# Kernel tuning notes

Measured on AMD Instinct MI355X. Metric: run time of the kernel, lower is better.

Reference implementation:

```python
import jax, jax.numpy as jnp
import numpy as np


def rational_hat(points, centers, radius):
    # points: [B, P, 2], centers: [K, 2], radius: [1]
    # L1 distance of each point to each center: [B, P, K]
    norm = jnp.abs(points[:, :, None, :] - centers[None, None, :, :]).sum(-1)
    r = jnp.abs(radius[0])
    val = 1.0 / (1.0 + norm) - 1.0 / (1.0 + jnp.abs(r - norm))
    return val.sum(axis=1)  # [B, K]


def setup_inputs() -> dict:
    key = jax.random.key(0)
    k1, k2, k3, k4, k5 = jax.random.split(key, 5)
    B, N0, N1, N2, K = 32, 20000, 10000, 10000, 64
    return {
        "beta_0_up": jax.random.uniform(k1, (B, N0, 2), dtype=jnp.float32),
        "beta_0_down": jax.random.uniform(k2, (B, N0, 2), dtype=jnp.float32),
        "beta0_ext": jax.random.uniform(k3, (B, N1, 2), dtype=jnp.float32),
        "beta1_ext": jax.random.uniform(k4, (B, N2, 2), dtype=jnp.float32),
        "centers": jax.random.uniform(k5, (K, 2), dtype=jnp.float32),
        "radius": jnp.full((1,), 0.1, dtype=jnp.float32),
    }


def reference(beta_0_up, beta_0_down, beta0_ext, beta1_ext, centers, radius):
    x0, y0 = beta0_ext[..., 0], beta0_ext[..., 1]
    x1, y1 = beta1_ext[..., 0], beta1_ext[..., 1]
    b0_1st = jnp.stack([x0, 1.0 - x0], axis=-1)  # [B, N1, 2]
    b0_2nd = jnp.stack([y0, 1.0 - y0], axis=-1)
    b1_1st = jnp.stack([x1, 1.0 - x1], axis=-1)  # [B, N2, 2]
    b1_2nd = jnp.stack([y1, 1.0 - y1], axis=-1)
    ph_down = jnp.concatenate([beta_0_down, b0_1st, b1_1st], axis=1)  # [B, P, 2]
    ph_up = jnp.concatenate([beta_0_up, b0_2nd, b1_2nd], axis=1)
    up_out = rational_hat(ph_up, centers, radius)    # [B, K]
    down_out = rational_hat(ph_down, centers, radius)
    tpl = -((up_out - down_out) ** 2).sum()
    x = jnp.concatenate([up_out, down_out], axis=1)  # [B, 2K]
    return (x, tpl)
```

## Files before the change

### kernel.cpp

```cpp
#include <hip/hip_runtime.h>

typedef float v2f __attribute__((ext_vector_type(2)));

#define NB 32
#define N0 20000
#define N1 10000
#define N2 10000
#define NT_A 157
#define KC_A 8
#define KC_B 16
#define NBINS 4096
#define SENT 3.0e4f

__global__ __launch_bounds__(256, 8) void hat_kernel(
    const float* __restrict__ up0, const float* __restrict__ down0,
    const float* __restrict__ ext0, const float* __restrict__ ext1,
    const float* __restrict__ centers, const float* __restrict__ radius,
    float* __restrict__ out)
{
    const int tid  = threadIdx.x;
    const int lane = tid & 63;
    const int wave = tid >> 6;
    const float r  = fabsf(radius[0]);

    __shared__ unsigned hist[NBINS];
    __shared__ float    red[4 * KC_B];

    if (blockIdx.x < 256) {
        const int id   = blockIdx.x;
        const int cc   = id & 3;
        const int side = (id >> 2) & 1;
        const int b    = id >> 3;
        const int cbase = cc * KC_B;

        for (int j = tid; j < NBINS; j += 256) hist[j] = 0;
        __syncthreads();

        const float2* e0 = (const float2*)(ext0 + (size_t)b * (N1*2));
        const float2* e1 = (const float2*)(ext1 + (size_t)b * (N2*2));
        for (int i = tid; i < N1; i += 256) {
            const float2 q0 = e0[i];
            const float2 q1 = e1[i];
            const float vv0 = (side == 0) ? q0.y : q0.x;
            const float vv1 = (side == 0) ? q1.y : q1.x;
            int b0 = (int)(vv0 * (float)NBINS);
            int b1 = (int)(vv1 * (float)NBINS);
            b0 = min(max(b0, 0), NBINS - 1);
            b1 = min(max(b1, 0), NBINS - 1);
            atomicAdd(&hist[b0], 1u);
            atomicAdd(&hist[b1], 1u);
        }
        __syncthreads();

        float Ak[KC_B], mk[KC_B];
        #pragma unroll
        for (int k = 0; k < KC_B; ++k) {
            const float cx = centers[2*(cbase+k)];
            const float cy = centers[2*(cbase+k)+1];
            Ak[k] = fabsf(1.0f - (cx + cy));
            mk[k] = 0.5f * (1.0f + (cx - cy));
        }

        float part[KC_B];
        #pragma unroll
        for (int k = 0; k < KC_B; ++k) part[k] = 0.f;

        #pragma unroll
        for (int jj = 0; jj < NBINS/256; ++jj) {
            const int j = jj*256 + tid;
            const float cntf = (float)hist[j];
            const float vvj  = ((float)j + 0.5f) * (1.0f/(float)NBINS);
            #pragma unroll
            for (int k = 0; k < KC_B; ++k) {
                const float s  = vvj - mk[k];
                const float tt = fmaxf(Ak[k], 2.0f*fabsf(s));
                const float d1 = 1.0f + tt;
                const float rn = r - tt;
                const float d2 = 1.0f + fabsf(rn);
                const float rc = __builtin_amdgcn_rcpf(d1 * d2);
                part[k] = fmaf(cntf * (d2 - d1), rc, part[k]);
            }
        }

        {
            #pragma unroll
            for (int k = 0; k < 8; ++k) {
                const bool hi = lane & 32;
                const float send = hi ? part[k]   : part[k+8];
                const float keep = hi ? part[k+8] : part[k];
                part[k] = keep + __shfl_xor(send, 32, 64);
            }
            #pragma unroll
            for (int k = 0; k < 4; ++k) {
                const bool hi = lane & 16;
                const float send = hi ? part[k]   : part[k+4];
                const float keep = hi ? part[k+4] : part[k];
                part[k] = keep + __shfl_xor(send, 16, 64);
            }
            #pragma unroll
            for (int k = 0; k < 2; ++k) {
                const bool hi = lane & 8;
                const float send = hi ? part[k]   : part[k+2];
                const float keep = hi ? part[k+2] : part[k];
                part[k] = keep + __shfl_xor(send, 8, 64);
            }
            {
                const bool hi = lane & 4;
                const float send = hi ? part[0] : part[1];
                const float keep = hi ? part[1] : part[0];
                part[0] = keep + __shfl_xor(send, 4, 64);
            }
            part[0] += __shfl_xor(part[0], 2, 64);
            part[0] += __shfl_xor(part[0], 1, 64);
        }
        if ((lane & 3) == 0) red[wave * KC_B + (lane >> 2)] = part[0];
        __syncthreads();
        if (tid < KC_B) {
            const float s = red[tid] + red[KC_B + tid] + red[2*KC_B + tid] + red[3*KC_B + tid];
            atomicAdd(&out[b*128 + side*64 + cbase + tid], s);
        }
        return;
    }

    const int bid    = blockIdx.x - 256;
    const int tchunk = bid & 3;
    const int cc     = (bid >> 2) & 7;
    const int side   = (bid >> 5) & 1;
    const int b      = bid >> 6;
    const int cbase  = cc * KC_A;

    v2f nuc[KC_A], nvc[KC_A];
    #pragma unroll
    for (int k = 0; k < KC_A; ++k) {
        const float cx = centers[2*(cbase+k)];
        const float cy = centers[2*(cbase+k)+1];
        nuc[k] = (v2f){-(cx + cy), -(cx + cy)};
        nvc[k] = (v2f){-(cx - cy), -(cx - cy)};
    }

    const float4* base0 = (const float4*)((side == 0 ? up0 : down0) + (size_t)b * (N0*2));

    v2f acc[KC_A];
    #pragma unroll
    for (int k = 0; k < KC_A; ++k) acc[k] = (v2f){0.f, 0.f};
    const v2f one2 = (v2f){1.f, 1.f};

    for (int t = tchunk*4 + wave; t < NT_A; t += 16) {
        const int i = t*64 + lane;
        v2f u_, v_;
        if (i < N0/2) {
            const float4 q = base0[i];
            u_ = (v2f){q.x + q.y, q.z + q.w};
            v_ = (v2f){q.x - q.y, q.z - q.w};
        } else {
            u_ = (v2f){SENT, SENT};
            v_ = (v2f){0.f, 0.f};
        }

        #pragma unroll
        for (int k = 0; k < KC_A; ++k) {
            const v2f du = u_ + nuc[k];
            const v2f dv = v_ + nvc[k];
            const float tt0 = fmaxf(fabsf(du.x), fabsf(dv.x));
            const float tt1 = fmaxf(fabsf(du.y), fabsf(dv.y));
            const v2f tt = (v2f){tt0, tt1};
            const v2f d1 = tt + one2;
            const float rn0 = r - tt0;
            const float rn1 = r - tt1;
            const v2f d2 = (v2f){1.f + fabsf(rn0), 1.f + fabsf(rn1)};
            const v2f dd  = d1 * d2;
            const v2f num = d2 - d1;
            const v2f rc  = (v2f){__builtin_amdgcn_rcpf(dd.x),
                                  __builtin_amdgcn_rcpf(dd.y)};
            acc[k] = __builtin_elementwise_fma(num, rc, acc[k]);
        }
    }

    float a1[KC_A];
    #pragma unroll
    for (int k = 0; k < KC_A; ++k) a1[k] = acc[k].x + acc[k].y;

    {
        #pragma unroll
        for (int k = 0; k < 4; ++k) {
            const bool hi = lane & 32;
            const float send = hi ? a1[k]   : a1[k+4];
            const float keep = hi ? a1[k+4] : a1[k];
            a1[k] = keep + __shfl_xor(send, 32, 64);
        }
        #pragma unroll
        for (int k = 0; k < 2; ++k) {
            const bool hi = lane & 16;
            const float send = hi ? a1[k]   : a1[k+2];
            const float keep = hi ? a1[k+2] : a1[k];
            a1[k] = keep + __shfl_xor(send, 16, 64);
        }
        {
            const bool hi = lane & 8;
            const float send = hi ? a1[0] : a1[1];
            const float keep = hi ? a1[1] : a1[0];
            a1[0] = keep + __shfl_xor(send, 8, 64);
        }
        a1[0] += __shfl_xor(a1[0], 4, 64);
        a1[0] += __shfl_xor(a1[0], 2, 64);
        a1[0] += __shfl_xor(a1[0], 1, 64);
    }
    if ((lane & 7) == 0) red[wave * KC_A + (lane >> 3)] = a1[0];
    __syncthreads();
    if (tid < KC_A) {
        const float s = red[tid] + red[KC_A + tid] + red[2*KC_A + tid] + red[3*KC_A + tid];
        atomicAdd(&out[b*128 + side*64 + cbase + tid], s);
    }
}

__global__ __launch_bounds__(256) void tpl_kernel(float* __restrict__ out)
{
    __shared__ float red[256];
    float s = 0.f;
    for (int i = threadIdx.x; i < NB*64; i += 256) {
        const int b = i >> 6, k = i & 63;
        const float d = out[b*128 + k] - out[b*128 + 64 + k];
        s = fmaf(d, d, s);
    }
    red[threadIdx.x] = s;
    __syncthreads();
    for (int w = 128; w > 0; w >>= 1) {
        if (threadIdx.x < w) red[threadIdx.x] += red[threadIdx.x + w];
        __syncthreads();
    }
    if (threadIdx.x == 0) out[NB*128] = -red[0];
}

extern "C" void kernel_launch(void* const* d_in, const int* in_sizes, int n_in,
                              void* d_out, int out_size, void* d_ws, size_t ws_size,
                              hipStream_t stream) {
    const float* up0     = (const float*)d_in[0];
    const float* down0   = (const float*)d_in[1];
    const float* ext0    = (const float*)d_in[2];
    const float* ext1    = (const float*)d_in[3];
    const float* centers = (const float*)d_in[4];
    const float* radius  = (const float*)d_in[5];
    float* out = (float*)d_out;

    hipMemsetAsync(out, 0, NB * 128 * sizeof(float), stream);

    hat_kernel<<<dim3(256 + 2048), dim3(256), 0, stream>>>(
        up0, down0, ext0, ext1, centers, radius, out);
    tpl_kernel<<<1, 256, 0, stream>>>(out);
}
```

Baseline: 107.6 us.

## Fuse tpl reduction into hat kernel via last-block counter and simplify hat math

Removes the separate tpl_kernel launch by having each block increment an atomic counter stored in the tpl output slot; the last block to finish computes the squared-difference reduction. The dense path now processes four points per lane with scalar math instead of v2f pairs, and rewrites the numerator algebraically as max(r-2t,-r) so d2 is derived from d1. This trims one kernel launch and a few ALU ops per point-center pair. In exchange it adds a global atomic, fences and an extra barrier to every block, and it relies on the counter's integer bits being overwritten correctly by the final float result.

```diff
diff --git a/kernel.cpp b/kernel.cpp
--- a/kernel.cpp
+++ b/kernel.cpp
@@ -1,15 +1,13 @@
 #include <hip/hip_runtime.h>
-
-typedef float v2f __attribute__((ext_vector_type(2)));
 
 #define NB 32
 #define N0 20000
 #define N1 10000
 #define N2 10000
-#define NT_A 157
 #define KC_A 8
 #define KC_B 16
 #define NBINS 4096
+#define NBLK_TOTAL (2048 + 256)
 #define SENT 3.0e4f
 
 __global__ __launch_bounds__(256, 8) void hat_kernel(
@@ -22,9 +20,11 @@
     const int lane = tid & 63;
     const int wave = tid >> 6;
     const float r  = fabsf(radius[0]);
+    const float nr = -r;
 
     __shared__ unsigned hist[NBINS];
     __shared__ float    red[4 * KC_B];
+    __shared__ int      is_last;
 
     if (blockIdx.x < 256) {
         const int id   = blockIdx.x;
@@ -119,116 +119,129 @@
             const float s = red[tid] + red[KC_B + tid] + red[2*KC_B + tid] + red[3*KC_B + tid];
             atomicAdd(&out[b*128 + side*64 + cbase + tid], s);
         }
-        return;
+    } else {
+        const int bid    = blockIdx.x - 256;
+        const int tchunk = bid & 3;
+        const int cc     = (bid >> 2) & 7;
+        const int side   = (bid >> 5) & 1;
+        const int b      = bid >> 6;
+        const int cbase  = cc * KC_A;
+
+        float uc[KC_A], vc[KC_A];
+        #pragma unroll
+        for (int k = 0; k < KC_A; ++k) {
+            const float cx = centers[2*(cbase+k)];
+            const float cy = centers[2*(cbase+k)+1];
+            uc[k] = cx + cy;
+            vc[k] = cx - cy;
+        }
+
+        const float4* base0 = (const float4*)((side == 0 ? up0 : down0) + (size_t)b * (N0*2));
+
+        float acc[KC_A][4];
+        #pragma unroll
+        for (int k = 0; k < KC_A; ++k)
+            #pragma unroll
+            for (int p = 0; p < 4; ++p) acc[k][p] = 0.f;
+
+        for (int t = tchunk*4 + wave; t < 79; t += 16) {
+            const int i0 = t*128 + 2*lane;
+            float u[4], v[4];
+            if (i0 < 10000) {
+                const float4 q0 = base0[i0];
+                const float4 q1 = base0[i0+1];
+                u[0] = q0.x + q0.y;  v[0] = q0.x - q0.y;
+                u[1] = q0.z + q0.w;  v[1] = q0.z - q0.w;
+                u[2] = q1.x + q1.y;  v[2] = q1.x - q1.y;
+                u[3] = q1.z + q1.w;  v[3] = q1.z - q1.w;
+            } else {
+                #pragma unroll
+                for (int p = 0; p < 4; ++p) { u[p] = SENT; v[p] = 0.f; }
+            }
+
+            #pragma unroll
+            for (int k = 0; k < KC_A; ++k) {
+                #pragma unroll
+                for (int p = 0; p < 4; ++p) {
+                    const float du = u[p] - uc[k];
+                    const float dv = v[p] - vc[k];
+                    const float tt = fmaxf(fabsf(du), fabsf(dv));
+                    const float d1 = 1.0f + tt;
+                    const float num = fmaxf(fmaf(-2.0f, tt, r), nr);
+                    const float d2 = d1 + num;
+                    const float rc = __builtin_amdgcn_rcpf(d1 * d2);
+                    acc[k][p] = fmaf(num, rc, acc[k][p]);
+                }
+            }
+        }
+
+        float a1[KC_A];
+        #pragma unroll
+        for (int k = 0; k < KC_A; ++k)
+            a1[k] = (acc[k][0] + acc[k][1]) + (acc[k][2] + acc[k][3]);
+
+        {
+            #pragma unroll
+            for (int k = 0; k < 4; ++k) {
+                const bool hi = lane & 32;
+                const float send = hi ? a1[k]   : a1[k+4];
+                const float keep = hi ? a1[k+4] : a1[k];
+                a1[k] = keep + __shfl_xor(send, 32, 64);
+            }
+            #pragma unroll
+            for (int k = 0; k < 2; ++k) {
+                const bool hi = lane & 16;
+                const float send = hi ? a1[k]   : a1[k+2];
+                const float keep = hi ? a1[k+2] : a1[k];
+                a1[k] = keep + __shfl_xor(send, 16, 64);
+            }
+            {
+                const bool hi = lane & 8;
+                const float send = hi ? a1[0] : a1[1];
+                const float keep = hi ? a1[1] : a1[0];
+                a1[0] = keep + __shfl_xor(send, 8, 64);
+            }
+            a1[0] += __shfl_xor(a1[0], 4, 64);
+            a1[0] += __shfl_xor(a1[0], 2, 64);
+            a1[0] += __shfl_xor(a1[0], 1, 64);
+        }
+        if ((lane & 7) == 0) red[wave * KC_A + (lane >> 3)] = a1[0];
+        __syncthreads();
+        if (tid < KC_A) {
+            const float s = red[tid] + red[KC_A + tid] + red[2*KC_A + tid] + red[3*KC_A + tid];
+            atomicAdd(&out[b*128 + side*64 + cbase + tid], s);
+        }
     }
 
-    const int bid    = blockIdx.x - 256;
-    const int tchunk = bid & 3;
-    const int cc     = (bid >> 2) & 7;
-    const int side   = (bid >> 5) & 1;
-    const int b      = bid >> 6;
-    const int cbase  = cc * KC_A;
-
-    v2f nuc[KC_A], nvc[KC_A];
-    #pragma unroll
-    for (int k = 0; k < KC_A; ++k) {
-        const float cx = centers[2*(cbase+k)];
-        const float cy = centers[2*(cbase+k)+1];
-        nuc[k] = (v2f){-(cx + cy), -(cx + cy)};
-        nvc[k] = (v2f){-(cx - cy), -(cx - cy)};
+    __syncthreads();
+    if (tid == 0) {
+        __threadfence();
+        const int old = atomicAdd((int*)&out[NB*128], 1);
+        is_last = (old == NBLK_TOTAL - 1);
     }
-
-    const float4* base0 = (const float4*)((side == 0 ? up0 : down0) + (size_t)b * (N0*2));
-
-    v2f acc[KC_A];
-    #pragma unroll
-    for (int k = 0; k < KC_A; ++k) acc[k] = (v2f){0.f, 0.f};
-    const v2f one2 = (v2f){1.f, 1.f};
-
-    for (int t = tchunk*4 + wave; t < NT_A; t += 16) {
-        const int i = t*64 + lane;
-        v2f u_, v_;
-        if (i < N0/2) {
-            const float4 q = base0[i];
-            u_ = (v2f){q.x + q.y, q.z + q.w};
-            v_ = (v2f){q.x - q.y, q.z - q.w};
-        } else {
-            u_ = (v2f){SENT, SENT};
-            v_ = (v2f){0.f, 0.f};
-        }
-
-        #pragma unroll
-        for (int k = 0; k < KC_A; ++k) {
-            const v2f du = u_ + nuc[k];
-            const v2f dv = v_ + nvc[k];
-            const float tt0 = fmaxf(fabsf(du.x), fabsf(dv.x));
-            const float tt1 = fmaxf(fabsf(du.y), fabsf(dv.y));
-            const v2f tt = (v2f){tt0, tt1};
-            const v2f d1 = tt + one2;
-            const float rn0 = r - tt0;
-            const float rn1 = r - tt1;
-            const v2f d2 = (v2f){1.f + fabsf(rn0), 1.f + fabsf(rn1)};
-            const v2f dd  = d1 * d2;
-            const v2f num = d2 - d1;
-            const v2f rc  = (v2f){__builtin_amdgcn_rcpf(dd.x),
-                                  __builtin_amdgcn_rcpf(dd.y)};
-            acc[k] = __builtin_elementwise_fma(num, rc, acc[k]);
+    __syncthreads();
+    if (is_last) {
+        if (tid == 0) __threadfence();
+        __syncthreads();
+        float s = 0.f;
+        for (int i = tid; i < NB*64; i += 256) {
+            const int bb = i >> 6, k = i & 63;
+            const float d = out[bb*128 + k] - out[bb*128 + 64 + k];
+            s = fmaf(d, d, s);
+        }
+        s += __shfl_xor(s, 32, 64);
+        s += __shfl_xor(s, 16, 64);
+        s += __shfl_xor(s, 8, 64);
+        s += __shfl_xor(s, 4, 64);
+        s += __shfl_xor(s, 2, 64);
+        s += __shfl_xor(s, 1, 64);
+        if (lane == 0) red[wave] = s;
+        __syncthreads();
+        if (tid == 0) {
+            const float tot = (red[0] + red[1]) + (red[2] + red[3]);
+            out[NB*128] = -tot;
         }
     }
-
-    float a1[KC_A];
-    #pragma unroll
-    for (int k = 0; k < KC_A; ++k) a1[k] = acc[k].x + acc[k].y;
-
-    {
-        #pragma unroll
-        for (int k = 0; k < 4; ++k) {
-            const bool hi = lane & 32;
-            const float send = hi ? a1[k]   : a1[k+4];
-            const float keep = hi ? a1[k+4] : a1[k];
-            a1[k] = keep + __shfl_xor(send, 32, 64);
-        }
-        #pragma unroll
-        for (int k = 0; k < 2; ++k) {
-            const bool hi = lane & 16;
-            const float send = hi ? a1[k]   : a1[k+2];
-            const float keep = hi ? a1[k+2] : a1[k];
-            a1[k] = keep + __shfl_xor(send, 16, 64);
-        }
-        {
-            const bool hi = lane & 8;
-            const float send = hi ? a1[0] : a1[1];
-            const float keep = hi ? a1[1] : a1[0];
-            a1[0] = keep + __shfl_xor(send, 8, 64);
-        }
-        a1[0] += __shfl_xor(a1[0], 4, 64);
-        a1[0] += __shfl_xor(a1[0], 2, 64);
-        a1[0] += __shfl_xor(a1[0], 1, 64);
-    }
-    if ((lane & 7) == 0) red[wave * KC_A + (lane >> 3)] = a1[0];
-    __syncthreads();
-    if (tid < KC_A) {
-        const float s = red[tid] + red[KC_A + tid] + red[2*KC_A + tid] + red[3*KC_A + tid];
-        atomicAdd(&out[b*128 + side*64 + cbase + tid], s);
-    }
-}
-
-__global__ __launch_bounds__(256) void tpl_kernel(float* __restrict__ out)
-{
-    __shared__ float red[256];
-    float s = 0.f;
-    for (int i = threadIdx.x; i < NB*64; i += 256) {
-        const int b = i >> 6, k = i & 63;
-        const float d = out[b*128 + k] - out[b*128 + 64 + k];
-        s = fmaf(d, d, s);
-    }
-    red[threadIdx.x] = s;
-    __syncthreads();
-    for (int w = 128; w > 0; w >>= 1) {
-        if (threadIdx.x < w) red[threadIdx.x] += red[threadIdx.x + w];
-        __syncthreads();
-    }
-    if (threadIdx.x == 0) out[NB*128] = -red[0];
 }
 
 extern "C" void kernel_launch(void* const* d_in, const int* in_sizes, int n_in,
@@ -242,9 +255,8 @@
     const float* radius  = (const float*)d_in[5];
     float* out = (float*)d_out;
 
-    hipMemsetAsync(out, 0, NB * 128 * sizeof(float), stream);
-
-    hat_kernel<<<dim3(256 + 2048), dim3(256), 0, stream>>>(
+    hipMemsetAsync(out, 0, (NB * 128 + 1) * sizeof(float), stream);
+
+    hat_kernel<<<dim3(NBLK_TOTAL), dim3(256), 0, stream>>>(
         up0, down0, ext0, ext1, centers, radius, out);
-    tpl_kernel<<<1, 256, 0, stream>>>(out);
 }
```

Result: slower. 151.4 us (+40.7%).
